# Kernel optimization log

Hardware: AMD Instinct MI355X
Metric: run time of the kernel (lower is better)

The kernel has to match this reference:

```python
import jax, jax.numpy as jnp
import numpy as np

N_NODES = 50000
N_EDGES = 400000
F_IN = 128
HID = 64
HEADS = 8
N_CLASSES = 16
NEG_SLOPE = 0.2  # PyG GATConv default negative_slope


def _glorot(key, shape):
    fan_in, fan_out = shape[0], shape[-1]
    lim = jnp.sqrt(6.0 / (fan_in + fan_out))
    return jax.random.uniform(key, shape, jnp.float32, -lim, lim)


def setup_inputs() -> dict:
    key = jax.random.key(0)
    ks = jax.random.split(key, 16)
    x = jax.random.normal(ks[0], (N_NODES, F_IN), jnp.float32)
    edge_index = jax.random.randint(ks[1], (2, N_EDGES), 0, N_NODES, jnp.int64)
    # layer 0: F_IN -> HEADS*HID (concat)
    W0 = _glorot(ks[2], (F_IN, HEADS * HID))
    a_s0 = _glorot(ks[3], (HEADS, HID))
    a_d0 = _glorot(ks[4], (HEADS, HID))
    b0 = jnp.zeros((HEADS * HID,), jnp.float32)
    # layer 1: HEADS*HID -> HEADS*HID (concat)
    W1 = _glorot(ks[5], (HEADS * HID, HEADS * HID))
    a_s1 = _glorot(ks[6], (HEADS, HID))
    a_d1 = _glorot(ks[7], (HEADS, HID))
    b1 = jnp.zeros((HEADS * HID,), jnp.float32)
    # final layer: HEADS*HID -> N_CLASSES, heads=1, concat=False (mean over heads)
    W2 = _glorot(ks[8], (HEADS * HID, 1 * N_CLASSES))
    a_s2 = _glorot(ks[9], (1, N_CLASSES))
    a_d2 = _glorot(ks[10], (1, N_CLASSES))
    b2 = jnp.zeros((N_CLASSES,), jnp.float32)
    return {"x": x, "edge_index": edge_index,
            "W0": W0, "a_s0": a_s0, "a_d0": a_d0, "b0": b0,
            "W1": W1, "a_s1": a_s1, "a_d1": a_d1, "b1": b1,
            "W2": W2, "a_s2": a_s2, "a_d2": a_d2, "b2": b2}


def gat_conv(x, src, dst, W, a_src, a_dst, b, num_nodes, concat):
    """One PyG-style GATConv (self-loops already in src/dst).
    x: [N, F_in]; W: [F_in, H*C]; a_src/a_dst: [H, C]; b: [H*C] or [C]."""
    H, C = a_src.shape
    h = (x @ W).reshape(num_nodes, H, C)                    # [N,H,C]
    al_s = jnp.einsum('nhc,hc->nh', h, a_src)               # [N,H]
    al_d = jnp.einsum('nhc,hc->nh', h, a_dst)               # [N,H]
    e = jax.nn.leaky_relu(al_s[src] + al_d[dst], NEG_SLOPE) # [E,H]
    # scatter-softmax over incoming edges of each destination node
    m = jax.ops.segment_max(e, dst, num_segments=num_nodes)  # [N,H]
    ex = jnp.exp(e - m[dst])
    denom = jax.ops.segment_sum(ex, dst, num_segments=num_nodes)
    alpha = ex / denom[dst]                                  # [E,H]
    out = jax.ops.segment_sum(alpha[:, :, None] * h[src], dst,
                              num_segments=num_nodes)        # [N,H,C]
    if concat:
        return out.reshape(num_nodes, H * C) + b
    return out.mean(axis=1) + b


def reference(x, edge_index, W0, a_s0, a_d0, b0, W1, a_s1, a_d1, b1,
              W2, a_s2, a_d2, b2):
    N = x.shape[0]
    # PyG GATConv adds self-loops by default
    loops = jnp.arange(N, dtype=edge_index.dtype)
    src = jnp.concatenate([edge_index[0], loops])
    dst = jnp.concatenate([edge_index[1], loops])
    h = gat_conv(x, src, dst, W0, a_s0, a_d0, b0, N, concat=True)
    h = jax.nn.elu(h)  # dropout is identity in eval mode
    h = gat_conv(h, src, dst, W1, a_s1, a_d1, b1, N, concat=True)
    h = jax.nn.elu(h)
    return gat_conv(h, src, dst, W2, a_s2, a_d2, b2, N, concat=False)
```

## Files before the change

kernel.cpp:

```cpp
#include <hip/hip_runtime.h>

#define N_NODES 50000
#define N_EDGES 400000
#define E_TOT   450000
#define NEG 0.2f
#define NB_SCAN ((N_NODES + 255) / 256)
#define MAXD 64

typedef unsigned short ushort_t;
typedef __attribute__((ext_vector_type(8))) _Float16 half8;
typedef __attribute__((ext_vector_type(4))) float  f32x4;
typedef __attribute__((ext_vector_type(8))) unsigned short ushort8;

__device__ __forceinline__ ushort_t f2h(float f){
    _Float16 h = (_Float16)f;
    union { _Float16 h; ushort_t u; } v; v.h = h; return v.u;
}
__device__ __forceinline__ float h_lo(unsigned u){
    union { unsigned u; _Float16 h[2]; } v; v.u = u; return (float)v.h[0];
}
__device__ __forceinline__ float h_hi(unsigned u){
    union { unsigned u; _Float16 h[2]; } v; v.u = u; return (float)v.h[1];
}
__device__ __forceinline__ void gload_lds16(const void* g, void* l){
    __builtin_amdgcn_global_load_lds((const __attribute__((address_space(1))) void*)g,
                                     (__attribute__((address_space(3))) void*)l, 16, 0, 0);
}
__device__ __forceinline__ int wave_incl_scan(int v, int lane){
    #pragma unroll
    for(int off = 1; off < 64; off <<= 1){
        int t = __shfl_up(v, off, 64);
        if(lane >= off) v += t;
    }
    return v;
}


__global__ void count_deg(const int* __restrict__ ei, int* __restrict__ deg){
    int e = blockIdx.x*256 + threadIdx.x;
    if(e >= E_TOT) return;
    int dst = (e < N_EDGES) ? ei[N_EDGES + e] : (e - N_EDGES);
    atomicAdd(&deg[dst], 1);
}

__global__ void deg_block_sum(const int* __restrict__ deg, int* __restrict__ bsum){
    int i = blockIdx.x*256 + threadIdx.x;
    int lane = threadIdx.x & 63, wave = threadIdx.x >> 6;
    int v = (i < N_NODES) ? deg[i] : 0;
    #pragma unroll
    for(int off = 1; off < 64; off <<= 1) v += __shfl_xor(v, off, 64);
    __shared__ int sw[4];
    if(lane == 0) sw[wave] = v;
    __syncthreads();
    if(threadIdx.x == 0) bsum[blockIdx.x] = sw[0] + sw[1] + sw[2] + sw[3];
}

__global__ void scan_apply(const int* __restrict__ bsum,
                           int* __restrict__ dw, int* __restrict__ rowptr){
    __shared__ int soff;
    __shared__ int sw[4];
    int i = blockIdx.x*256 + threadIdx.x;
    int lane = threadIdx.x & 63, wave = threadIdx.x >> 6;
    if(wave == 0){
        int s = 0;
        for(int j = lane; j < (int)blockIdx.x; j += 64) s += bsum[j];
        #pragma unroll
        for(int off = 1; off < 64; off <<= 1) s += __shfl_xor(s, off, 64);
        if(lane == 0) soff = s;
    }
    int v = (i < N_NODES) ? dw[i] : 0;
    int incl = wave_incl_scan(v, lane);
    if(lane == 63) sw[wave] = incl;
    __syncthreads();
    int add = soff;
    for(int w = 0; w < wave; w++) add += sw[w];
    int excl = incl - v + add;
    if(i < N_NODES){ rowptr[i] = excl; dw[i] = excl; }
    if(i == N_NODES-1) rowptr[N_NODES] = excl + v;
}

__global__ void scatter_edges(const int* __restrict__ ei, int* __restrict__ wofs,
                              int* __restrict__ csr){
    int e = blockIdx.x*256 + threadIdx.x;
    if(e >= E_TOT) return;
    int src, dst;
    if(e < N_EDGES){ src = ei[e]; dst = ei[N_EDGES + e]; }
    else { src = dst = e - N_EDGES; }
    int pos = atomicAdd(&wofs[dst], 1);
    csr[pos] = src;
}


__global__ void cvt_all(const float* __restrict__ x, const float* __restrict__ W0,
                        const float* __restrict__ W1, const float* __restrict__ W2,
                        ushort_t* __restrict__ xbf, ushort_t* __restrict__ W0t,
                        ushort_t* __restrict__ W1t, ushort_t* __restrict__ W2t,
                        int* __restrict__ wofs){
    int i = blockIdx.x*256 + threadIdx.x;
    if(i < N_NODES*128) xbf[i] = f2h(x[i]);
    if(i < 512*128){ int n = i >> 7, k = i & 127; W0t[i] = f2h(W0[(size_t)k*512 + n]); }
    if(i < 512*512){ int n = i >> 9, k = i & 511; W1t[i] = f2h(W1[(size_t)k*512 + n]); }
    if(i < 16*512){ int n = i >> 9, k = i & 511; W2t[i] = f2h(W2[(size_t)k*16 + n]); }
    if(i < N_NODES) wofs[i] = 0;
}


template<int K>
__global__ __launch_bounds__(256) void gemm_bt(const ushort_t* __restrict__ A,
                                               const ushort_t* __restrict__ Bt,
                                               ushort_t* __restrict__ Cb,
                                               const float* __restrict__ a_s,
                                               const float* __restrict__ a_d,
                                               float* __restrict__ als,
                                               float* __restrict__ ald, int M){
    __shared__ ushort_t As[128*32];
    __shared__ ushort_t Bs[128*32];
    int tid  = threadIdx.x;
    int wave = tid >> 6, lane = tid & 63;
    int wm = wave & 1, wn = wave >> 1;
    int row0 = blockIdx.y * 128;
    int col0 = blockIdx.x * 128;

    f32x4 acc[4][4] = {};

    int lrow = lane >> 2;
    int lchk = (lane & 3) * 8;

    for(int kt = 0; kt < K; kt += 32){
        #pragma unroll
        for(int s = 0; s < 2; s++){
            int seg = wave*2 + s;
            int ar = row0 + seg*16 + lrow;
            ar = ar < M ? ar : M-1;
            gload_lds16(A  + (size_t)ar*K + kt + lchk, As + seg*512);
            int br = col0 + seg*16 + lrow;
            gload_lds16(Bt + (size_t)br*K + kt + lchk, Bs + seg*512);
        }
        __syncthreads();

        half8 a[4], b[4];
        int fm = lane & 15, fq = (lane >> 4) * 8;
        #pragma unroll
        for(int t = 0; t < 4; t++){
            a[t] = *(const half8*)&As[(wm*64 + t*16 + fm)*32 + fq];
            b[t] = *(const half8*)&Bs[(wn*64 + t*16 + fm)*32 + fq];
        }
        #pragma unroll
        for(int i = 0; i < 4; i++)
            #pragma unroll
            for(int j = 0; j < 4; j++)
                acc[i][j] = __builtin_amdgcn_mfma_f32_16x16x32_f16(a[i], b[j], acc[i][j], 0, 0, 0);
        __syncthreads();
    }

    int cm = (lane >> 4) * 4, cn = lane & 15;
    int head = (col0 + wn*64) >> 6;
    float as_[4], ad_[4];
    #pragma unroll
    for(int j = 0; j < 4; j++){
        int c = head*64 + cn + j*16;
        as_[j] = a_s[c]; ad_[j] = a_d[c];
    }
    #pragma unroll
    for(int i = 0; i < 4; i++){
        #pragma unroll
        for(int p = 0; p < 4; p++){
            int r = row0 + wm*64 + i*16 + cm + p;
            float ps = 0.f, pd = 0.f;
            if(r < M){
                ushort_t* cp = &Cb[(size_t)r*512 + col0 + wn*64 + cn];
                #pragma unroll
                for(int j = 0; j < 4; j++){
                    float v = acc[i][j][p];
                    cp[j*16] = f2h(v);
                    ps += v*as_[j]; pd += v*ad_[j];
                }
            }
            #pragma unroll
            for(int off = 1; off < 16; off <<= 1){
                ps += __shfl_xor(ps, off);
                pd += __shfl_xor(pd, off);
            }
            if(cn == 0 && r < M){ als[r*8 + head] = ps; ald[r*8 + head] = pd; }
        }
    }
}


__global__ __launch_bounds__(512, 2) void gemm_bt8(const ushort_t* __restrict__ A,
                                                   const ushort_t* __restrict__ Bt,
                                                   ushort_t* __restrict__ Cb,
                                                   const float* __restrict__ a_s,
                                                   const float* __restrict__ a_d,
                                                   float* __restrict__ als,
                                                   float* __restrict__ ald, int M){
    extern __shared__ ushort_t lds[];
    const int K = 512;
    int tid = threadIdx.x, wave = tid >> 6, lane = tid & 63;
    int wm = wave >> 2, wn = wave & 3;
    int row0 = blockIdx.y * 256;
    int col0 = blockIdx.x * 256;

    int lr = lane >> 3;
    int cs8 = ((lane & 7) ^ lr) << 3;
    int arows[4], brows[4];
    #pragma unroll
    for(int i = 0; i < 4; i++){
        int r = row0 + (wave << 5) + (i << 3) + lr;
        arows[i] = r < M ? r : M-1;
        brows[i] = col0 + (wave << 5) + (i << 3) + lr;
    }

    int l15 = lane & 15, fq = lane >> 4;
    int xr = (lane & 7) << 4;
    int xco0 = ((fq << 4)      ) ^ xr;
    int xco1 = (64 | (fq << 4)) ^ xr;

    f32x4 acc[8][4] = {};

    auto stage = [&](int nb, int kt, int i){
        ushort_t* la = lds + nb*16384 + (wave << 11) + (i << 9);
        ushort_t* lb = lds + 32768 + nb*16384 + (wave << 11) + (i << 9);
        gload_lds16(A  + (size_t)arows[i]*K + kt + cs8, la);
        gload_lds16(Bt + (size_t)brows[i]*K + kt + cs8, lb);
    };

    #pragma unroll
    for(int i = 0; i < 4; i++) stage(0, 0, i);

    for(int it = 0; it < 8; ++it){
        int b = it & 1;
        asm volatile("s_waitcnt vmcnt(0)" ::: "memory");
        __builtin_amdgcn_s_barrier();
        const char* Ac = (const char*)(lds + b*16384);
        const char* Bc = (const char*)(lds + 32768 + b*16384);
        #pragma unroll
        for(int p = 0; p < 4; ++p){
            if(it < 7) stage(b ^ 1, (it + 1) << 6, p);
            half8 aF[2][2], bF[4][2];
            #pragma unroll
            for(int m2 = 0; m2 < 2; m2++){
                int ro = (((wm << 7) + (((p << 1) | m2) << 4) + l15)) << 7;
                aF[m2][0] = *(const half8*)(Ac + ro + xco0);
                aF[m2][1] = *(const half8*)(Ac + ro + xco1);
            }
            #pragma unroll
            for(int nj = 0; nj < 4; nj++){
                int ro = (((wn << 6) + (nj << 4) + l15)) << 7;
                bF[nj][0] = *(const half8*)(Bc + ro + xco0);
                bF[nj][1] = *(const half8*)(Bc + ro + xco1);
            }
            __builtin_amdgcn_s_barrier();
            __builtin_amdgcn_s_setprio(1);
            #pragma unroll
            for(int m2 = 0; m2 < 2; m2++)
                #pragma unroll
                for(int nj = 0; nj < 4; nj++){
                    acc[(p<<1)|m2][nj] = __builtin_amdgcn_mfma_f32_16x16x32_f16(aF[m2][0], bF[nj][0], acc[(p<<1)|m2][nj], 0, 0, 0);
                    acc[(p<<1)|m2][nj] = __builtin_amdgcn_mfma_f32_16x16x32_f16(aF[m2][1], bF[nj][1], acc[(p<<1)|m2][nj], 0, 0, 0);
                }
            __builtin_amdgcn_s_setprio(0);
            __builtin_amdgcn_s_barrier();
        }
    }

    int head = (col0 >> 6) + wn;
    float asv[4], adv[4];
    #pragma unroll
    for(int nj = 0; nj < 4; nj++){
        int c = (head << 6) + (nj << 4) + l15;
        asv[nj] = a_s[c]; adv[nj] = a_d[c];
    }
    #pragma unroll
    for(int mi = 0; mi < 8; mi++){
        #pragma unroll
        for(int p2 = 0; p2 < 4; p2++){
            int r = row0 + (wm << 7) + (mi << 4) + (fq << 2) + p2;
            float ps = 0.f, pd = 0.f;
            if(r < M){
                ushort_t* cp = &Cb[(size_t)r*512 + (head << 6) + l15];
                #pragma unroll
                for(int nj = 0; nj < 4; nj++){
                    float v = acc[mi][nj][p2];
                    cp[nj << 4] = f2h(v);
                    ps += v*asv[nj]; pd += v*adv[nj];
                }
            }
            #pragma unroll
            for(int off = 1; off < 16; off <<= 1){
                ps += __shfl_xor(ps, off);
                pd += __shfl_xor(pd, off);
            }
            if(l15 == 0 && r < M){ als[r*8 + head] = ps; ald[r*8 + head] = pd; }
        }
    }
}


__global__ __launch_bounds__(256) void attn_agg(const ushort_t* __restrict__ h,
        const float* __restrict__ als, const float* __restrict__ ald,
        const int* __restrict__ rowptr, const int* __restrict__ csr,
        const float* __restrict__ bias, ushort_t* __restrict__ out){
    __shared__ float sm[4][8], sd[4][8];
    __shared__ float sex[4][MAXD][8];
    int wv = threadIdx.x >> 6, lane = threadIdx.x & 63;
    int n = blockIdx.x*4 + wv;
    int start = rowptr[n], end = rowptr[n+1];

    int hd = lane & 7, e8 = lane >> 3;
    float aldv = ald[n*8 + hd];
    float lmax = -1e30f;
    for(int idx = start + e8; idx < end; idx += 8){
        int e = idx - start;
        int src = csr[idx];
        float v = als[src*8 + hd] + aldv;
        v = v > 0.f ? v : NEG*v;
        if(e < MAXD) sex[wv][e][hd] = v;
        lmax = fmaxf(lmax, v);
    }
    for(int off = 8; off < 64; off <<= 1) lmax = fmaxf(lmax, __shfl_xor(lmax, off));
    float lsum = 0.f;
    for(int idx = start + e8; idx < end; idx += 8){
        int e = idx - start;
        float v;
        if(e < MAXD) v = sex[wv][e][hd];
        else { int src = csr[idx]; v = als[src*8 + hd] + aldv; v = v > 0.f ? v : NEG*v; }
        float ex = __expf(v - lmax);
        if(e < MAXD) sex[wv][e][hd] = ex;
        lsum += ex;
    }
    for(int off = 8; off < 64; off <<= 1) lsum += __shfl_xor(lsum, off);
    if(lane < 8){ sm[wv][hd] = lmax; sd[wv][hd] = 1.f / lsum; }
    __syncthreads();

    int head = lane >> 3;
    float inv = sd[wv][head];
    float acc[8] = {};

    int cnt = end - start;
    int nmain = cnt < MAXD ? cnt : MAXD;
    int mend = start + nmain;
    int last = mend - 1;
    for(int idx = start; idx < mend; idx += 8){
        int ss[8]; uint4 pp[8]; float ee[8];
        #pragma unroll
        for(int k = 0; k < 8; k++){
            int j = idx + k;
            ss[k] = csr[j <= last ? j : last];
        }
        #pragma unroll
        for(int k = 0; k < 8; k++)
            pp[k] = *(const uint4*)&h[(size_t)ss[k]*512 + lane*8];
        #pragma unroll
        for(int k = 0; k < 8; k++){
            int j = idx + k;
            ee[k] = (j < mend) ? sex[wv][j-start][head] : 0.f;
        }
        #pragma unroll
        for(int k = 0; k < 8; k++){
            acc[0] += ee[k]*h_lo(pp[k].x); acc[1] += ee[k]*h_hi(pp[k].x);
            acc[2] += ee[k]*h_lo(pp[k].y); acc[3] += ee[k]*h_hi(pp[k].y);
            acc[4] += ee[k]*h_lo(pp[k].z); acc[5] += ee[k]*h_hi(pp[k].z);
            acc[6] += ee[k]*h_lo(pp[k].w); acc[7] += ee[k]*h_hi(pp[k].w);
        }
    }
    if(mend < end){
        float m = sm[wv][head];
        float aldn = ald[n*8 + head];
        for(int idx = mend; idx < end; idx++){
            int src = csr[idx];
            float v = als[src*8 + head] + aldn;
            v = v > 0.f ? v : NEG*v;
            float e0 = __expf(v - m);
            uint4 p = *(const uint4*)&h[(size_t)src*512 + lane*8];
            acc[0] += e0*h_lo(p.x); acc[1] += e0*h_hi(p.x);
            acc[2] += e0*h_lo(p.y); acc[3] += e0*h_hi(p.y);
            acc[4] += e0*h_lo(p.z); acc[5] += e0*h_hi(p.z);
            acc[6] += e0*h_lo(p.w); acc[7] += e0*h_hi(p.w);
        }
    }

    ushort8 o;
    #pragma unroll
    for(int j = 0; j < 8; j++){
        float v = acc[j]*inv + bias[lane*8 + j];
        v = v > 0.f ? v : (__expf(v) - 1.f);
        o[j] = f2h(v);
    }
    *(ushort8*)&out[(size_t)n*512 + lane*8] = o;
}


__global__ __launch_bounds__(256) void gemm2_mfma(const ushort_t* __restrict__ A,
                                                  const ushort_t* __restrict__ W2t,
                                                  const float* __restrict__ a_s2,
                                                  const float* __restrict__ a_d2,
                                                  float* __restrict__ C,
                                                  float* __restrict__ als,
                                                  float* __restrict__ ald){
    int wave = threadIdx.x >> 6, lane = threadIdx.x & 63;
    long row0 = (long)(blockIdx.x*4 + wave)*16;
    int fr = lane & 15, fq = lane >> 4;
    long ar = row0 + fr;
    if(ar > N_NODES-1) ar = N_NODES-1;
    const ushort_t* ap = A + ar*512 + fq*8;
    const ushort_t* bp = W2t + (size_t)fr*512 + fq*8;
    f32x4 acc = {};
    #pragma unroll
    for(int kt = 0; kt < 512; kt += 32){
        half8 a = *(const half8*)(ap + kt);
        half8 b = *(const half8*)(bp + kt);
        acc = __builtin_amdgcn_mfma_f32_16x16x32_f16(a, b, acc, 0, 0, 0);
    }
    float as_ = a_s2[fr], ad_ = a_d2[fr];
    #pragma unroll
    for(int p = 0; p < 4; p++){
        long r = row0 + fq*4 + p;
        float v = acc[p];
        float ps = v*as_, pd = v*ad_;
        #pragma unroll
        for(int off = 1; off < 16; off <<= 1){
            ps += __shfl_xor(ps, off);
            pd += __shfl_xor(pd, off);
        }
        if(r < N_NODES){
            C[r*16 + fr] = v;
            if(fr == 0){ als[r] = ps; ald[r] = pd; }
        }
    }
}

__global__ __launch_bounds__(256) void attn_agg2(const float* __restrict__ h2,
        const float* __restrict__ als, const float* __restrict__ ald,
        const int* __restrict__ rowptr, const int* __restrict__ csr,
        const float* __restrict__ b2, float* __restrict__ out){
    __shared__ float sex2[16][MAXD+1];
    int wv = threadIdx.x >> 6, lane = threadIdx.x & 63;
    int q = lane >> 4, c = lane & 15;
    int slot = wv*4 + q;
    int n = blockIdx.x*16 + slot;
    int start = rowptr[n], end = rowptr[n+1];
    float aldv = ald[n];
    int cnt = end - start;
    int nmain = cnt < MAXD ? cnt : MAXD;
    int mend = start + nmain;

    float lmax = -1e30f;
    for(int idx = start + c; idx < end; idx += 16){
        int e = idx - start;
        float v = als[csr[idx]] + aldv; v = v > 0.f ? v : NEG*v;
        if(e < MAXD) sex2[slot][e] = v;
        lmax = fmaxf(lmax, v);
    }
    #pragma unroll
    for(int off = 1; off < 16; off <<= 1) lmax = fmaxf(lmax, __shfl_xor(lmax, off));
    float lsum = 0.f;
    for(int idx = start + c; idx < end; idx += 16){
        int e = idx - start;
        float v;
        if(e < MAXD) v = sex2[slot][e];
        else { v = als[csr[idx]] + aldv; v = v > 0.f ? v : NEG*v; }
        float ex = __expf(v - lmax);
        if(e < MAXD) sex2[slot][e] = ex;
        lsum += ex;
    }
    #pragma unroll
    for(int off = 1; off < 16; off <<= 1) lsum += __shfl_xor(lsum, off);
    float inv = 1.f / lsum;

    float acc = 0.f;
    for(int idx = start; idx < mend; idx++){
        int src = csr[idx];
        float ex = sex2[slot][idx - start];
        acc += ex * h2[(size_t)src*16 + c];
    }
    for(int idx = mend; idx < end; idx++){
        int src = csr[idx];
        float v = als[src] + aldv; v = v > 0.f ? v : NEG*v;
        acc += __expf(v - lmax) * h2[(size_t)src*16 + c];
    }
    out[(size_t)n*16 + c] = acc*inv + b2[c];
}


extern "C" void kernel_launch(void* const* d_in, const int* in_sizes, int n_in,
                              void* d_out, int out_size, void* d_ws, size_t ws_size,
                              hipStream_t stream) {
    const float* x    = (const float*)d_in[0];
    const int*   ei   = (const int*)  d_in[1];
    const float* W0   = (const float*)d_in[2];
    const float* a_s0 = (const float*)d_in[3];
    const float* a_d0 = (const float*)d_in[4];
    const float* b0   = (const float*)d_in[5];
    const float* W1   = (const float*)d_in[6];
    const float* a_s1 = (const float*)d_in[7];
    const float* a_d1 = (const float*)d_in[8];
    const float* b1   = (const float*)d_in[9];
    const float* W2   = (const float*)d_in[10];
    const float* a_s2 = (const float*)d_in[11];
    const float* a_d2 = (const float*)d_in[12];
    const float* b2   = (const float*)d_in[13];
    float* out = (float*)d_out;

    char* w = (char*)d_ws;
    auto alloc = [&](size_t bytes){ void* p = (void*)w; w += (bytes + 255) & ~(size_t)255; return p; };
    int*      rowptr = (int*)     alloc((N_NODES+1)*sizeof(int));
    int*      wofs   = (int*)     alloc(N_NODES*sizeof(int));
    int*      bsum   = (int*)     alloc(NB_SCAN*sizeof(int));
    int*      csr    = (int*)     alloc(E_TOT*sizeof(int));
    float*    als    = (float*)   alloc((size_t)N_NODES*8*sizeof(float));
    float*    ald    = (float*)   alloc((size_t)N_NODES*8*sizeof(float));
    ushort_t* hb     = (ushort_t*)alloc((size_t)N_NODES*512*sizeof(ushort_t));
    ushort_t* hbf    = (ushort_t*)alloc((size_t)N_NODES*512*sizeof(ushort_t));
    ushort_t* xbf    = (ushort_t*)alloc((size_t)N_NODES*128*sizeof(ushort_t));
    ushort_t* W0t    = (ushort_t*)alloc((size_t)512*128*sizeof(ushort_t));
    ushort_t* W1t    = (ushort_t*)alloc((size_t)512*512*sizeof(ushort_t));
    ushort_t* W2t    = (ushort_t*)alloc((size_t)16*512*sizeof(ushort_t));
    float*    h2     = (float*)   alloc((size_t)N_NODES*16*sizeof(float));

    (void)hipFuncSetAttribute((const void*)gemm_bt8,
                              hipFuncAttributeMaxDynamicSharedMemorySize, 131072);

    cvt_all<<<(N_NODES*128+255)/256, 256, 0, stream>>>(x, W0, W1, W2, xbf, W0t, W1t, W2t, wofs);

    count_deg<<<(E_TOT+255)/256, 256, 0, stream>>>(ei, wofs);
    deg_block_sum<<<NB_SCAN, 256, 0, stream>>>(wofs, bsum);
    scan_apply<<<NB_SCAN, 256, 0, stream>>>(bsum, wofs, rowptr);
    scatter_edges<<<(E_TOT+255)/256, 256, 0, stream>>>(ei, wofs, csr);

    gemm_bt<128><<<dim3(4, (N_NODES+127)/128), 256, 0, stream>>>(xbf, W0t, hb, a_s0, a_d0, als, ald, N_NODES);
    attn_agg<<<N_NODES/4, 256, 0, stream>>>(hb, als, ald, rowptr, csr, b0, hbf);

    gemm_bt8<<<dim3(2, (N_NODES+255)/256), 512, 131072, stream>>>(hbf, W1t, hb, a_s1, a_d1, als, ald, N_NODES);
    attn_agg<<<N_NODES/4, 256, 0, stream>>>(hb, als, ald, rowptr, csr, b1, hbf);

    gemm2_mfma<<<(N_NODES+63)/64, 256, 0, stream>>>(hbf, W2t, a_s2, a_d2, h2, als, ald);
    attn_agg2<<<N_NODES/16, 256, 0, stream>>>(h2, als, ald, rowptr, csr, b2, out);
}
```

Before: 426.6 us.

## Fuse CSR build into conversion, template big GEMM for layer 0, fold final GEMM into aggregation

Degree counting moves into the conversion kernel. The two-kernel scan is replaced by a single kernel that scans each wave and claims row ranges with an atomic, so rows are no longer in order and separate start/end arrays replace rowptr. Layer 0 now uses the pipelined 256-row GEMM (templated on K) instead of the smaller 128-tile kernel, and the stage issue pattern is reshuffled. The final 512x16 projection and its attention logits are computed inside the layer-1 aggregation kernel, which removes the separate gemm2 launch and one re-read of the hidden features, at the cost of per-wave shuffle reductions.

```diff
diff --git a/kernel.cpp b/kernel.cpp
--- a/kernel.cpp
+++ b/kernel.cpp
@@ -36,47 +36,35 @@
 }
 
 
-__global__ void count_deg(const int* __restrict__ ei, int* __restrict__ deg){
-    int e = blockIdx.x*256 + threadIdx.x;
-    if(e >= E_TOT) return;
-    int dst = (e < N_EDGES) ? ei[N_EDGES + e] : (e - N_EDGES);
-    atomicAdd(&deg[dst], 1);
-}
-
-__global__ void deg_block_sum(const int* __restrict__ deg, int* __restrict__ bsum){
+__global__ void cvt_all(const float* __restrict__ x, const float* __restrict__ W0,
+                        const float* __restrict__ W1, const float* __restrict__ W2,
+                        const int* __restrict__ ei,
+                        ushort_t* __restrict__ xbf, ushort_t* __restrict__ W0t,
+                        ushort_t* __restrict__ W1t, ushort_t* __restrict__ W2t,
+                        int* __restrict__ deg){
     int i = blockIdx.x*256 + threadIdx.x;
-    int lane = threadIdx.x & 63, wave = threadIdx.x >> 6;
-    int v = (i < N_NODES) ? deg[i] : 0;
-    #pragma unroll
-    for(int off = 1; off < 64; off <<= 1) v += __shfl_xor(v, off, 64);
-    __shared__ int sw[4];
-    if(lane == 0) sw[wave] = v;
-    __syncthreads();
-    if(threadIdx.x == 0) bsum[blockIdx.x] = sw[0] + sw[1] + sw[2] + sw[3];
-}
-
-__global__ void scan_apply(const int* __restrict__ bsum,
-                           int* __restrict__ dw, int* __restrict__ rowptr){
-    __shared__ int soff;
-    __shared__ int sw[4];
+    if(i < N_NODES*128) xbf[i] = f2h(x[i]);
+    if(i < 512*128){ int n = i >> 7, k = i & 127; W0t[i] = f2h(W0[(size_t)k*512 + n]); }
+    if(i < 512*512){ int n = i >> 9, k = i & 511; W1t[i] = f2h(W1[(size_t)k*512 + n]); }
+    if(i < 16*512){ int n = i >> 9, k = i & 511; W2t[i] = f2h(W2[(size_t)k*16 + n]); }
+    if(i < E_TOT){
+        int dst = (i < N_EDGES) ? ei[N_EDGES + i] : (i - N_EDGES);
+        atomicAdd(&deg[dst], 1);
+    }
+}
+
+
+__global__ void alloc_rows(int* __restrict__ wofs, int* __restrict__ rs, int* __restrict__ re){
     int i = blockIdx.x*256 + threadIdx.x;
-    int lane = threadIdx.x & 63, wave = threadIdx.x >> 6;
-    if(wave == 0){
-        int s = 0;
-        for(int j = lane; j < (int)blockIdx.x; j += 64) s += bsum[j];
-        #pragma unroll
-        for(int off = 1; off < 64; off <<= 1) s += __shfl_xor(s, off, 64);
-        if(lane == 0) soff = s;
-    }
-    int v = (i < N_NODES) ? dw[i] : 0;
-    int incl = wave_incl_scan(v, lane);
-    if(lane == 63) sw[wave] = incl;
-    __syncthreads();
-    int add = soff;
-    for(int w = 0; w < wave; w++) add += sw[w];
-    int excl = incl - v + add;
-    if(i < N_NODES){ rowptr[i] = excl; dw[i] = excl; }
-    if(i == N_NODES-1) rowptr[N_NODES] = excl + v;
+    int lane = threadIdx.x & 63;
+    int d = (i < N_NODES) ? wofs[i] : 0;
+    int incl = wave_incl_scan(d, lane);
+    int tot = __shfl(incl, 63);
+    int base;
+    if(lane == 63) base = atomicAdd(&wofs[N_NODES], tot);
+    base = __shfl(base, 63);
+    int start = base + incl - d;
+    if(i < N_NODES){ rs[i] = start; re[i] = start + d; wofs[i] = start; }
 }
 
 __global__ void scatter_edges(const int* __restrict__ ei, int* __restrict__ wofs,
@@ -91,102 +79,7 @@
 }
 
 
-__global__ void cvt_all(const float* __restrict__ x, const float* __restrict__ W0,
-                        const float* __restrict__ W1, const float* __restrict__ W2,
-                        ushort_t* __restrict__ xbf, ushort_t* __restrict__ W0t,
-                        ushort_t* __restrict__ W1t, ushort_t* __restrict__ W2t,
-                        int* __restrict__ wofs){
-    int i = blockIdx.x*256 + threadIdx.x;
-    if(i < N_NODES*128) xbf[i] = f2h(x[i]);
-    if(i < 512*128){ int n = i >> 7, k = i & 127; W0t[i] = f2h(W0[(size_t)k*512 + n]); }
-    if(i < 512*512){ int n = i >> 9, k = i & 511; W1t[i] = f2h(W1[(size_t)k*512 + n]); }
-    if(i < 16*512){ int n = i >> 9, k = i & 511; W2t[i] = f2h(W2[(size_t)k*16 + n]); }
-    if(i < N_NODES) wofs[i] = 0;
-}
-
-
 template<int K>
-__global__ __launch_bounds__(256) void gemm_bt(const ushort_t* __restrict__ A,
-                                               const ushort_t* __restrict__ Bt,
-                                               ushort_t* __restrict__ Cb,
-                                               const float* __restrict__ a_s,
-                                               const float* __restrict__ a_d,
-                                               float* __restrict__ als,
-                                               float* __restrict__ ald, int M){
-    __shared__ ushort_t As[128*32];
-    __shared__ ushort_t Bs[128*32];
-    int tid  = threadIdx.x;
-    int wave = tid >> 6, lane = tid & 63;
-    int wm = wave & 1, wn = wave >> 1;
-    int row0 = blockIdx.y * 128;
-    int col0 = blockIdx.x * 128;
-
-    f32x4 acc[4][4] = {};
-
-    int lrow = lane >> 2;
-    int lchk = (lane & 3) * 8;
-
-    for(int kt = 0; kt < K; kt += 32){
-        #pragma unroll
-        for(int s = 0; s < 2; s++){
-            int seg = wave*2 + s;
-            int ar = row0 + seg*16 + lrow;
-            ar = ar < M ? ar : M-1;
-            gload_lds16(A  + (size_t)ar*K + kt + lchk, As + seg*512);
-            int br = col0 + seg*16 + lrow;
-            gload_lds16(Bt + (size_t)br*K + kt + lchk, Bs + seg*512);
-        }
-        __syncthreads();
-
-        half8 a[4], b[4];
-        int fm = lane & 15, fq = (lane >> 4) * 8;
-        #pragma unroll
-        for(int t = 0; t < 4; t++){
-            a[t] = *(const half8*)&As[(wm*64 + t*16 + fm)*32 + fq];
-            b[t] = *(const half8*)&Bs[(wn*64 + t*16 + fm)*32 + fq];
-        }
-        #pragma unroll
-        for(int i = 0; i < 4; i++)
-            #pragma unroll
-            for(int j = 0; j < 4; j++)
-                acc[i][j] = __builtin_amdgcn_mfma_f32_16x16x32_f16(a[i], b[j], acc[i][j], 0, 0, 0);
-        __syncthreads();
-    }
-
-    int cm = (lane >> 4) * 4, cn = lane & 15;
-    int head = (col0 + wn*64) >> 6;
-    float as_[4], ad_[4];
-    #pragma unroll
-    for(int j = 0; j < 4; j++){
-        int c = head*64 + cn + j*16;
-        as_[j] = a_s[c]; ad_[j] = a_d[c];
-    }
-    #pragma unroll
-    for(int i = 0; i < 4; i++){
-        #pragma unroll
-        for(int p = 0; p < 4; p++){
-            int r = row0 + wm*64 + i*16 + cm + p;
-            float ps = 0.f, pd = 0.f;
-            if(r < M){
-                ushort_t* cp = &Cb[(size_t)r*512 + col0 + wn*64 + cn];
-                #pragma unroll
-                for(int j = 0; j < 4; j++){
-                    float v = acc[i][j][p];
-                    cp[j*16] = f2h(v);
-                    ps += v*as_[j]; pd += v*ad_[j];
-                }
-            }
-            #pragma unroll
-            for(int off = 1; off < 16; off <<= 1){
-                ps += __shfl_xor(ps, off);
-                pd += __shfl_xor(pd, off);
-            }
-            if(cn == 0 && r < M){ als[r*8 + head] = ps; ald[r*8 + head] = pd; }
-        }
-    }
-}
-
-
 __global__ __launch_bounds__(512, 2) void gemm_bt8(const ushort_t* __restrict__ A,
                                                    const ushort_t* __restrict__ Bt,
                                                    ushort_t* __restrict__ Cb,
@@ -195,7 +88,7 @@
                                                    float* __restrict__ als,
                                                    float* __restrict__ ald, int M){
     extern __shared__ ushort_t lds[];
-    const int K = 512;
+    constexpr int NT = K / 64;
     int tid = threadIdx.x, wave = tid >> 6, lane = tid & 63;
     int wm = wave >> 2, wn = wave & 3;
     int row0 = blockIdx.y * 256;
@@ -228,7 +121,7 @@
     #pragma unroll
     for(int i = 0; i < 4; i++) stage(0, 0, i);
 
-    for(int it = 0; it < 8; ++it){
+    for(int it = 0; it < NT; ++it){
         int b = it & 1;
         asm volatile("s_waitcnt vmcnt(0)" ::: "memory");
         __builtin_amdgcn_s_barrier();
@@ -236,7 +129,10 @@
         const char* Bc = (const char*)(lds + 32768 + b*16384);
         #pragma unroll
         for(int p = 0; p < 4; ++p){
-            if(it < 7) stage(b ^ 1, (it + 1) << 6, p);
+            if(it < NT-1 && p < 2){
+                stage(b ^ 1, (it + 1) << 6, 2*p);
+                stage(b ^ 1, (it + 1) << 6, 2*p + 1);
+            }
             half8 aF[2][2], bF[4][2];
             #pragma unroll
             for(int m2 = 0; m2 < 2; m2++){
@@ -297,15 +193,20 @@
 }
 
 
+template<bool F2>
 __global__ __launch_bounds__(256) void attn_agg(const ushort_t* __restrict__ h,
         const float* __restrict__ als, const float* __restrict__ ald,
-        const int* __restrict__ rowptr, const int* __restrict__ csr,
-        const float* __restrict__ bias, ushort_t* __restrict__ out){
+        const int* __restrict__ rs, const int* __restrict__ re,
+        const int* __restrict__ csr,
+        const float* __restrict__ bias, ushort_t* __restrict__ out,
+        const ushort_t* __restrict__ W2t, const float* __restrict__ a_s2,
+        const float* __restrict__ a_d2, float* __restrict__ h2,
+        float* __restrict__ als2, float* __restrict__ ald2){
     __shared__ float sm[4][8], sd[4][8];
     __shared__ float sex[4][MAXD][8];
     int wv = threadIdx.x >> 6, lane = threadIdx.x & 63;
     int n = blockIdx.x*4 + wv;
-    int start = rowptr[n], end = rowptr[n+1];
+    int start = rs[n], end = re[n];
 
     int hd = lane & 7, e8 = lane >> 3;
     float aldv = ald[n*8 + hd];
@@ -380,66 +281,47 @@
         }
     }
 
+    float vv[8];
     ushort8 o;
     #pragma unroll
     for(int j = 0; j < 8; j++){
         float v = acc[j]*inv + bias[lane*8 + j];
         v = v > 0.f ? v : (__expf(v) - 1.f);
+        vv[j] = v;
         o[j] = f2h(v);
     }
     *(ushort8*)&out[(size_t)n*512 + lane*8] = o;
-}
-
-
-__global__ __launch_bounds__(256) void gemm2_mfma(const ushort_t* __restrict__ A,
-                                                  const ushort_t* __restrict__ W2t,
-                                                  const float* __restrict__ a_s2,
-                                                  const float* __restrict__ a_d2,
-                                                  float* __restrict__ C,
-                                                  float* __restrict__ als,
-                                                  float* __restrict__ ald){
-    int wave = threadIdx.x >> 6, lane = threadIdx.x & 63;
-    long row0 = (long)(blockIdx.x*4 + wave)*16;
-    int fr = lane & 15, fq = lane >> 4;
-    long ar = row0 + fr;
-    if(ar > N_NODES-1) ar = N_NODES-1;
-    const ushort_t* ap = A + ar*512 + fq*8;
-    const ushort_t* bp = W2t + (size_t)fr*512 + fq*8;
-    f32x4 acc = {};
-    #pragma unroll
-    for(int kt = 0; kt < 512; kt += 32){
-        half8 a = *(const half8*)(ap + kt);
-        half8 b = *(const half8*)(bp + kt);
-        acc = __builtin_amdgcn_mfma_f32_16x16x32_f16(a, b, acc, 0, 0, 0);
-    }
-    float as_ = a_s2[fr], ad_ = a_d2[fr];
-    #pragma unroll
-    for(int p = 0; p < 4; p++){
-        long r = row0 + fq*4 + p;
-        float v = acc[p];
-        float ps = v*as_, pd = v*ad_;
-        #pragma unroll
-        for(int off = 1; off < 16; off <<= 1){
-            ps += __shfl_xor(ps, off);
-            pd += __shfl_xor(pd, off);
-        }
-        if(r < N_NODES){
-            C[r*16 + fr] = v;
-            if(fr == 0){ als[r] = ps; ald[r] = pd; }
-        }
+
+    if constexpr (F2){
+        float ps = 0.f, pd = 0.f, yval = 0.f;
+        #pragma unroll
+        for(int c = 0; c < 16; c++){
+            half8 wvv = *(const half8*)&W2t[c*512 + lane*8];
+            float yc = vv[0]*(float)wvv[0] + vv[1]*(float)wvv[1]
+                     + vv[2]*(float)wvv[2] + vv[3]*(float)wvv[3]
+                     + vv[4]*(float)wvv[4] + vv[5]*(float)wvv[5]
+                     + vv[6]*(float)wvv[6] + vv[7]*(float)wvv[7];
+            #pragma unroll
+            for(int off = 1; off < 64; off <<= 1) yc += __shfl_xor(yc, off);
+            ps += yc * a_s2[c]; pd += yc * a_d2[c];
+            if(lane == c) yval = yc;
+        }
+        if(lane < 16) h2[(size_t)n*16 + lane] = yval;
+        if(lane == 0){ als2[n] = ps; ald2[n] = pd; }
     }
 }
 
 __global__ __launch_bounds__(256) void attn_agg2(const float* __restrict__ h2,
         const float* __restrict__ als, const float* __restrict__ ald,
-        const int* __restrict__ rowptr, const int* __restrict__ csr,
+        const int* __restrict__ rs, const int* __restrict__ re,
+        const int* __restrict__ csr,
         const float* __restrict__ b2, float* __restrict__ out){
     __shared__ float sex2[16][MAXD+1];
     int wv = threadIdx.x >> 6, lane = threadIdx.x & 63;
     int q = lane >> 4, c = lane & 15;
     int slot = wv*4 + q;
     int n = blockIdx.x*16 + slot;
-    int start = rowptr[n], end = rowptr[n+1];
+    int start = rs[n], end = re[n];
     float aldv = ald[n];
     int cnt = end - start;
     int nmain = cnt < MAXD ? cnt : MAXD;
@@ -504,12 +386,14 @@
 
     char* w = (char*)d_ws;
     auto alloc = [&](size_t bytes){ void* p = (void*)w; w += (bytes + 255) & ~(size_t)255; return p; };
-    int*      rowptr = (int*)     alloc((N_NODES+1)*sizeof(int));
-    int*      wofs   = (int*)     alloc(N_NODES*sizeof(int));
-    int*      bsum   = (int*)     alloc(NB_SCAN*sizeof(int));
+    int*      rs     = (int*)     alloc(N_NODES*sizeof(int));
+    int*      re     = (int*)     alloc(N_NODES*sizeof(int));
+    int*      wofs   = (int*)     alloc((N_NODES+1)*sizeof(int));
     int*      csr    = (int*)     alloc(E_TOT*sizeof(int));
     float*    als    = (float*)   alloc((size_t)N_NODES*8*sizeof(float));
     float*    ald    = (float*)   alloc((size_t)N_NODES*8*sizeof(float));
+    float*    als2   = (float*)   alloc((size_t)N_NODES*sizeof(float));
+    float*    ald2   = (float*)   alloc((size_t)N_NODES*sizeof(float));
     ushort_t* hb     = (ushort_t*)alloc((size_t)N_NODES*512*sizeof(ushort_t));
     ushort_t* hbf    = (ushort_t*)alloc((size_t)N_NODES*512*sizeof(ushort_t));
     ushort_t* xbf    = (ushort_t*)alloc((size_t)N_NODES*128*sizeof(ushort_t));
@@ -518,22 +402,24 @@
     ushort_t* W2t    = (ushort_t*)alloc((size_t)16*512*sizeof(ushort_t));
     float*    h2     = (float*)   alloc((size_t)N_NODES*16*sizeof(float));
 
-    (void)hipFuncSetAttribute((const void*)gemm_bt8,
+    (void)hipFuncSetAttribute((const void*)gemm_bt8<128>,
                               hipFuncAttributeMaxDynamicSharedMemorySize, 131072);
-
-    cvt_all<<<(N_NODES*128+255)/256, 256, 0, stream>>>(x, W0, W1, W2, xbf, W0t, W1t, W2t, wofs);
-
-    count_deg<<<(E_TOT+255)/256, 256, 0, stream>>>(ei, wofs);
-    deg_block_sum<<<NB_SCAN, 256, 0, stream>>>(wofs, bsum);
-    scan_apply<<<NB_SCAN, 256, 0, stream>>>(bsum, wofs, rowptr);
+    (void)hipFuncSetAttribute((const void*)gemm_bt8<512>,
+                              hipFuncAttributeMaxDynamicSharedMemorySize, 131072);
+
+    hipMemsetAsync(wofs, 0, (N_NODES+1)*sizeof(int), stream);
+    cvt_all<<<(N_NODES*128+255)/256, 256, 0, stream>>>(x, W0, W1, W2, ei, xbf, W0t, W1t, W2t, wofs);
+
+    alloc_rows<<<NB_SCAN, 256, 0, stream>>>(wofs, rs, re);
     scatter_edges<<<(E_TOT+255)/256, 256, 0, stream>>>(ei, wofs, csr);
 
-    gemm_bt<128><<<dim3(4, (N_NODES+127)/128), 256, 0, stream>>>(xbf, W0t, hb, a_s0, a_d0, als, ald, N_NODES);
-    attn_agg<<<N_NODES/4, 256, 0, stream>>>(hb, als, ald, rowptr, csr, b0, hbf);
-
-    gemm_bt8<<<dim3(2, (N_NODES+255)/256), 512, 131072, stream>>>(hbf, W1t, hb, a_s1, a_d1, als, ald, N_NODES);
-    attn_agg<<<N_NODES/4, 256, 0, stream>>>(hb, als, ald, rowptr, csr, b1, hbf);
-
-    gemm2_mfma<<<(N_NODES+63)/64, 256, 0, stream>>>(hbf, W2t, a_s2, a_d2, h2, als, ald);
-    attn_agg2<<<N_NODES/16, 256, 0, stream>>>(h2, als, ald, rowptr, csr, b2, out);
-}
+    gemm_bt8<128><<<dim3(2, (N_NODES+255)/256), 512, 131072, stream>>>(xbf, W0t, hb, a_s0, a_d0, als, ald, N_NODES);
+    attn_agg<false><<<N_NODES/4, 256, 0, stream>>>(hb, als, ald, rs, re, csr, b0, hbf,
+                                                   nullptr, nullptr, nullptr, nullptr, nullptr, nullptr);
+
+    gemm_bt8<512><<<dim3(2, (N_NODES+255)/256), 512, 131072, stream>>>(hbf, W1t, hb, a_s1, a_d1, als, ald, N_NODES);
+    attn_agg<true><<<N_NODES/4, 256, 0, stream>>>(hb, als, ald, rs, re, csr, b1, hbf,
+                                                  W2t, a_s2, a_d2, h2, als2, ald2);
+
+    attn_agg2<<<N_NODES/16, 256, 0, stream>>>(h2, als2, ald2, rs, re, csr, b2, out);
+}
```

New measurement: 442.9 us. 3.8% more time.

## Fuse degree count into conversion, remap GEMM blocks, and reschedule LDS staging

Applied to the files above, without the earlier changes.

Degree counting now happens inside the conversion kernel and the offsets buffer is cleared with a memset, which removes one kernel launch. The layer-1 GEMM is templated on K and uses a 1D grid whose block IDs are remapped into contiguous chunks of 8 groups, probably to keep neighbouring row tiles on the same XCD for L2 reuse. The next tile's global-to-LDS staging is now issued as two pairs in the first two sub-steps, not one per sub-step. The final layer also gets its own attention-score buffers instead of reusing the layer-0/1 ones.

```diff
diff --git a/kernel.cpp b/kernel.cpp
--- a/kernel.cpp
+++ b/kernel.cpp
@@ -36,12 +36,23 @@
 }
 
 
-__global__ void count_deg(const int* __restrict__ ei, int* __restrict__ deg){
-    int e = blockIdx.x*256 + threadIdx.x;
-    if(e >= E_TOT) return;
-    int dst = (e < N_EDGES) ? ei[N_EDGES + e] : (e - N_EDGES);
-    atomicAdd(&deg[dst], 1);
-}
+__global__ void cvt_all(const float* __restrict__ x, const float* __restrict__ W0,
+                        const float* __restrict__ W1, const float* __restrict__ W2,
+                        const int* __restrict__ ei,
+                        ushort_t* __restrict__ xbf, ushort_t* __restrict__ W0t,
+                        ushort_t* __restrict__ W1t, ushort_t* __restrict__ W2t,
+                        int* __restrict__ deg){
+    int i = blockIdx.x*256 + threadIdx.x;
+    if(i < N_NODES*128) xbf[i] = f2h(x[i]);
+    if(i < 512*128){ int n = i >> 7, k = i & 127; W0t[i] = f2h(W0[(size_t)k*512 + n]); }
+    if(i < 512*512){ int n = i >> 9, k = i & 511; W1t[i] = f2h(W1[(size_t)k*512 + n]); }
+    if(i < 16*512){ int n = i >> 9, k = i & 511; W2t[i] = f2h(W2[(size_t)k*16 + n]); }
+    if(i < E_TOT){
+        int dst = (i < N_EDGES) ? ei[N_EDGES + i] : (i - N_EDGES);
+        atomicAdd(&deg[dst], 1);
+    }
+}
+
 
 __global__ void deg_block_sum(const int* __restrict__ deg, int* __restrict__ bsum){
     int i = blockIdx.x*256 + threadIdx.x;
@@ -88,20 +99,6 @@
     else { src = dst = e - N_EDGES; }
     int pos = atomicAdd(&wofs[dst], 1);
     csr[pos] = src;
-}
-
-
-__global__ void cvt_all(const float* __restrict__ x, const float* __restrict__ W0,
-                        const float* __restrict__ W1, const float* __restrict__ W2,
-                        ushort_t* __restrict__ xbf, ushort_t* __restrict__ W0t,
-                        ushort_t* __restrict__ W1t, ushort_t* __restrict__ W2t,
-                        int* __restrict__ wofs){
-    int i = blockIdx.x*256 + threadIdx.x;
-    if(i < N_NODES*128) xbf[i] = f2h(x[i]);
-    if(i < 512*128){ int n = i >> 7, k = i & 127; W0t[i] = f2h(W0[(size_t)k*512 + n]); }
-    if(i < 512*512){ int n = i >> 9, k = i & 511; W1t[i] = f2h(W1[(size_t)k*512 + n]); }
-    if(i < 16*512){ int n = i >> 9, k = i & 511; W2t[i] = f2h(W2[(size_t)k*16 + n]); }
-    if(i < N_NODES) wofs[i] = 0;
 }
 
 
@@ -187,6 +184,7 @@
 }
 
 
+template<int K>
 __global__ __launch_bounds__(512, 2) void gemm_bt8(const ushort_t* __restrict__ A,
                                                    const ushort_t* __restrict__ Bt,
                                                    ushort_t* __restrict__ Cb,
@@ -195,11 +193,16 @@
                                                    float* __restrict__ als,
                                                    float* __restrict__ ald, int M){
     extern __shared__ ushort_t lds[];
-    const int K = 512;
+    constexpr int NT = K / 64;
     int tid = threadIdx.x, wave = tid >> 6, lane = tid & 63;
     int wm = wave >> 2, wn = wave & 3;
-    int row0 = blockIdx.y * 256;
-    int col0 = blockIdx.x * 256;
+
+    int s = blockIdx.x, nb = gridDim.x;
+    int cc = s & 7, kk = s >> 3;
+    int q = nb >> 3, rr = nb & 7;
+    int t = (cc < rr ? cc*(q+1) : rr*(q+1) + (cc-rr)*q) + kk;
+    int row0 = (t >> 1) * 256;
+    int col0 = (t & 1) * 256;
 
     int lr = lane >> 3;
     int cs8 = ((lane & 7) ^ lr) << 3;
@@ -218,9 +221,9 @@
 
     f32x4 acc[8][4] = {};
 
-    auto stage = [&](int nb, int kt, int i){
-        ushort_t* la = lds + nb*16384 + (wave << 11) + (i << 9);
-        ushort_t* lb = lds + 32768 + nb*16384 + (wave << 11) + (i << 9);
+    auto stage = [&](int nbuf, int kt, int i){
+        ushort_t* la = lds + nbuf*16384 + (wave << 11) + (i << 9);
+        ushort_t* lb = lds + 32768 + nbuf*16384 + (wave << 11) + (i << 9);
         gload_lds16(A  + (size_t)arows[i]*K + kt + cs8, la);
         gload_lds16(Bt + (size_t)brows[i]*K + kt + cs8, lb);
     };
@@ -228,7 +231,7 @@
     #pragma unroll
     for(int i = 0; i < 4; i++) stage(0, 0, i);
 
-    for(int it = 0; it < 8; ++it){
+    for(int it = 0; it < NT; ++it){
         int b = it & 1;
         asm volatile("s_waitcnt vmcnt(0)" ::: "memory");
         __builtin_amdgcn_s_barrier();
@@ -236,7 +239,10 @@
         const char* Bc = (const char*)(lds + 32768 + b*16384);
         #pragma unroll
         for(int p = 0; p < 4; ++p){
-            if(it < 7) stage(b ^ 1, (it + 1) << 6, p);
+            if(it < NT-1 && p < 2){
+                stage(b ^ 1, (it + 1) << 6, 2*p);
+                stage(b ^ 1, (it + 1) << 6, 2*p + 1);
+            }
             half8 aF[2][2], bF[4][2];
             #pragma unroll
             for(int m2 = 0; m2 < 2; m2++){
@@ -505,11 +511,13 @@
     char* w = (char*)d_ws;
     auto alloc = [&](size_t bytes){ void* p = (void*)w; w += (bytes + 255) & ~(size_t)255; return p; };
     int*      rowptr = (int*)     alloc((N_NODES+1)*sizeof(int));
-    int*      wofs   = (int*)     alloc(N_NODES*sizeof(int));
+    int*      wofs   = (int*)     alloc((N_NODES+1)*sizeof(int));
     int*      bsum   = (int*)     alloc(NB_SCAN*sizeof(int));
     int*      csr    = (int*)     alloc(E_TOT*sizeof(int));
     float*    als    = (float*)   alloc((size_t)N_NODES*8*sizeof(float));
     float*    ald    = (float*)   alloc((size_t)N_NODES*8*sizeof(float));
+    float*    als2   = (float*)   alloc((size_t)N_NODES*sizeof(float));
+    float*    ald2   = (float*)   alloc((size_t)N_NODES*sizeof(float));
     ushort_t* hb     = (ushort_t*)alloc((size_t)N_NODES*512*sizeof(ushort_t));
     ushort_t* hbf    = (ushort_t*)alloc((size_t)N_NODES*512*sizeof(ushort_t));
     ushort_t* xbf    = (ushort_t*)alloc((size_t)N_NODES*128*sizeof(ushort_t));
@@ -518,12 +526,14 @@
     ushort_t* W2t    = (ushort_t*)alloc((size_t)16*512*sizeof(ushort_t));
     float*    h2     = (float*)   alloc((size_t)N_NODES*16*sizeof(float));
 
-    (void)hipFuncSetAttribute((const void*)gemm_bt8,
+    const int NBLK = 2 * ((N_NODES + 255) / 256);
+
+    (void)hipFuncSetAttribute((const void*)gemm_bt8<512>,
                               hipFuncAttributeMaxDynamicSharedMemorySize, 131072);
 
-    cvt_all<<<(N_NODES*128+255)/256, 256, 0, stream>>>(x, W0, W1, W2, xbf, W0t, W1t, W2t, wofs);
-
-    count_deg<<<(E_TOT+255)/256, 256, 0, stream>>>(ei, wofs);
+    hipMemsetAsync(wofs, 0, (N_NODES+1)*sizeof(int), stream);
+    cvt_all<<<(N_NODES*128+255)/256, 256, 0, stream>>>(x, W0, W1, W2, ei, xbf, W0t, W1t, W2t, wofs);
+
     deg_block_sum<<<NB_SCAN, 256, 0, stream>>>(wofs, bsum);
     scan_apply<<<NB_SCAN, 256, 0, stream>>>(bsum, wofs, rowptr);
     scatter_edges<<<(E_TOT+255)/256, 256, 0, stream>>>(ei, wofs, csr);
@@ -531,9 +541,9 @@
     gemm_bt<128><<<dim3(4, (N_NODES+127)/128), 256, 0, stream>>>(xbf, W0t, hb, a_s0, a_d0, als, ald, N_NODES);
     attn_agg<<<N_NODES/4, 256, 0, stream>>>(hb, als, ald, rowptr, csr, b0, hbf);
 
-    gemm_bt8<<<dim3(2, (N_NODES+255)/256), 512, 131072, stream>>>(hbf, W1t, hb, a_s1, a_d1, als, ald, N_NODES);
+    gemm_bt8<512><<<NBLK, 512, 131072, stream>>>(hbf, W1t, hb, a_s1, a_d1, als, ald, N_NODES);
     attn_agg<<<N_NODES/4, 256, 0, stream>>>(hb, als, ald, rowptr, csr, b1, hbf);
 
-    gemm2_mfma<<<(N_NODES+63)/64, 256, 0, stream>>>(hbf, W2t, a_s2, a_d2, h2, als, ald);
-    attn_agg2<<<N_NODES/16, 256, 0, stream>>>(h2, als, ald, rowptr, csr, b2, out);
-}
+    gemm2_mfma<<<(N_NODES+63)/64, 256, 0, stream>>>(hbf, W2t, a_s2, a_d2, h2, als2, ald2);
+    attn_agg2<<<N_NODES/16, 256, 0, stream>>>(h2, als2, ald2, rowptr, csr, b2, out);
+}
```

Result: no change. 424.3 us (-0.5%).
